# Kernel tuning notes

Hardware: AMD Instinct MI355X
Metric: run time of the kernel (lower is better)

## Reference

```python
import jax, jax.numpy as jnp
import numpy as np

N2 = 128      # time horizon (days)
M = 16384     # number of regions / batched chains
START = 6     # seeding window (days with externally seeded cases)


def setup_inputs() -> dict:
    key = jax.random.key(0)
    k0, k1, k2, k3, k4 = jax.random.split(key, 5)
    # reproduction numbers R_t in [0, 2)
    rt = jax.random.uniform(k0, (N2, M), dtype=jnp.float32) * 2.0
    deaths_gt = jax.random.uniform(k1, (N2, M), dtype=jnp.float32)
    # serial-interval distribution (positive, sums to 1 so the recurrence stays bounded)
    si_raw = jax.random.uniform(k2, (N2,), dtype=jnp.float32)
    SI = si_raw / jnp.sum(si_raw)
    f_raw = jax.random.uniform(k3, (N2, M), dtype=jnp.float32)
    f = f_raw / jnp.sum(f_raw, axis=0, keepdims=True) * 0.01
    # seeded cases for the first START days
    seed = jax.random.uniform(k4, (START, M), dtype=jnp.float32)
    return {"rt": rt, "deaths_gt": deaths_gt, "SI": SI, "f": f,
            "seed": seed, "start": START}


def _predict_cases(rt, SI, seed, start):
    # prediction[i, m] = rt[i, m] * sum_{j < i} prediction[j, m] * SI[i - j]
    # sequential triangular recurrence over time -> lax.scan with full carry.
    n2, m = rt.shape
    idx = jnp.arange(n2)
    pred0 = jnp.zeros((n2, m), rt.dtype).at[:start].set(seed)

    def step(pred, i):
        d = i - idx                                   # SI lag for each j
        w = jnp.where(d > 0, SI[jnp.clip(d, 0, n2 - 1)], 0.0)  # [N2], zero for j >= i
        conv = w @ pred                               # [M]
        row = jnp.where(i >= start, rt[i] * conv, pred[i])
        return pred.at[i].set(row), None

    pred, _ = jax.lax.scan(step, pred0, jnp.arange(n2))
    return pred


def _predict_deaths(pred, f, start):
    # E_deaths[i, m] = sum_{j <= i-2} pred[j, m] * f[i-j, m]
    # = causal per-region convolution with lags d = i-j >= 2 (so zero f[0], f[1]).
    n2, m = pred.shape
    f_eff = f.at[:2].set(0.0)
    conv = jax.vmap(lambda p, k: jnp.convolve(p, k)[:n2],
                    in_axes=1, out_axes=1)(pred, f_eff)   # [N2, M]
    i = jnp.arange(n2)[:, None]
    # rows before `start` are untouched by the loop (0), row 0 is set to 1e-9
    return jnp.where(i >= start, conv, jnp.where(i == 0, 1e-9, 0.0))


def reference(rt, deaths_gt, SI, f, seed, start):
    cases_pred = _predict_cases(rt, SI, seed, start)
    deaths_pred = _predict_deaths(cases_pred, f, start)
    return jnp.mean((deaths_pred - deaths_gt) ** 2)  # nn.MSELoss
```

## Files before the change

### kernel.cpp

```cpp
#include <hip/hip_runtime.h>

#define N2 128
#define MM 16384
#define START 6
#define TC 64
#define W 8
#define BT (TC * W)


__global__ __launch_bounds__(BT) void npi_fused(
    const float* __restrict__ rt, const float* __restrict__ dgt,
    const float* __restrict__ si, const float* __restrict__ f,
    const float* __restrict__ seed, float* __restrict__ out)
{
    __shared__ float predT[N2 * TC];
    __shared__ float red[8 * 16 * TC];
    float* si_s = &red[7 * 16 * TC];
    float* lred = &red[7 * 16 * TC + N2];

    const int t = threadIdx.x;
    const int c = t & 63;
    const int w = t >> 6;
    const int m = blockIdx.x * TC + c;

    if (t < N2) si_s[t] = si[t];
    __syncthreads();

    float sr[16];
#pragma unroll
    for (int k = 1; k < 16; ++k) sr[k] = si_s[k];

    if (w == 7) {
        float v[16];
#pragma unroll
        for (int k = 0; k < 16; ++k) {
            if (k < START) {
                v[k] = seed[k * MM + m];
            } else {
                float s = 0.f;
#pragma unroll
                for (int kk = 0; kk < 16; ++kk)
                    if (kk < k) s += v[kk] * sr[k - kk];
                v[k] = rt[k * MM + m] * s;
            }
            predT[k * TC + c] = v[k];
        }
    }
    __syncthreads();

    for (int b = 1; b < 8; ++b) {
        const int i0 = b << 4;
        float r16[16];
        if (w == 7) {
#pragma unroll
            for (int k = 0; k < 16; ++k) r16[k] = rt[(i0 + k) * MM + m];
        } else if (w < b) {
            const int j0 = w << 4;
            const int D0 = i0 - j0 - 15;
            float c16[16];
#pragma unroll
            for (int e = 0; e < 16; ++e) c16[(e + 1) & 15] = si_s[D0 + e];
            float acc[16];
#pragma unroll
            for (int k = 0; k < 16; ++k) acc[k] = 0.f;
#pragma unroll
            for (int s = 0; s < 16; ++s) {
                float p = predT[((j0 + 15 - s) << 6) + c];
#pragma unroll
                for (int k = 0; k < 16; ++k)
                    acc[k] += p * c16[(s + k + 1) & 15];
                if (s < 15) c16[(s + 1) & 15] = si_s[D0 + 16 + s];
            }
#pragma unroll
            for (int k = 0; k < 16; ++k)
                red[(((w << 4) + k) << 6) + c] = acc[k];
        }
        __syncthreads();

#pragma unroll
        for (int e2 = 0; e2 < 2; ++e2) {
            int e = t + (e2 << 9);
            int k = e >> 6, c2 = e & 63;
            float tot = 0.f;
            for (int ww = 0; ww < b; ++ww)
                tot += red[(((ww << 4) + k) << 6) + c2];
            predT[((i0 + k) << 6) + c2] = tot;
        }
        __syncthreads();

        if (w == 7) {
            float v[16];
#pragma unroll
            for (int k = 0; k < 16; ++k) {
                float s = predT[((i0 + k) << 6) + c];
#pragma unroll
                for (int kk = 0; kk < 16; ++kk)
                    if (kk < k) s += v[kk] * sr[k - kk];
                v[k] = r16[k] * s;
                predT[((i0 + k) << 6) + c] = v[k];
            }
        }
        __syncthreads();
    }

#pragma unroll
    for (int q = 0; q < 16; ++q) {
        int d = w + (q << 3);
        red[(d << 6) + c] = f[d * MM + m];
    }
    __syncthreads();

    float lsum = 0.f;
    if (w == 0) {
        float d0 = 1e-9f - dgt[m];
        lsum = d0 * d0;
#pragma unroll
        for (int i = 1; i < START; ++i) {
            float di = dgt[i * MM + m];
            lsum += di * di;
        }
    }

#pragma unroll
    for (int half = 0; half < 2; ++half) {
        const int n = half ? (15 - w) : w;
        const int i0 = START + (n << 3);
        float acc8[8];
#pragma unroll
        for (int k = 0; k < 8; ++k) acc8[k] = 0.f;

        const int J = (i0 - 1) & ~7;
        const int jend = (i0 + 5 < 125) ? (i0 + 5) : 125;
        for (int j = J; j <= jend; ++j) {
            float pv = predT[(j << 6) + c];
#pragma unroll
            for (int k = 0; k < 8; ++k) {
                int d = i0 + k - j;
                if (d >= 2 && (i0 + k) < N2)
                    acc8[k] += pv * red[(d << 6) + c];
            }
        }
        if (J > 0) {
            float c8[8];
            const int d0f = i0 - J + 1;
#pragma unroll
            for (int k = 0; k < 8; ++k) c8[k] = red[((d0f + k) << 6) + c];
            for (int j8 = J - 8; j8 >= 0; j8 -= 8) {
                const int dbase = i0 - j8 - 7;
#pragma unroll
                for (int s = 0; s < 8; ++s) {
                    float pv = predT[((j8 + 7 - s) << 6) + c];
#pragma unroll
                    for (int k = 0; k < 8; ++k)
                        acc8[k] += pv * c8[(s + k) & 7];
                    int dr = dbase + s + 8;
                    if (dr > N2 - 1) dr = N2 - 1;
                    c8[s] = red[(dr << 6) + c];
                }
            }
        }
#pragma unroll
        for (int k = 0; k < 8; ++k) {
            int i = i0 + k;
            if (i < N2) {
                float diff = acc8[k] - dgt[i * MM + m];
                lsum += diff * diff;
            }
        }
    }

#pragma unroll
    for (int off = 32; off > 0; off >>= 1)
        lsum += __shfl_down(lsum, off, 64);
    __syncthreads();
    if (c == 0) lred[w] = lsum;
    __syncthreads();
    if (t == 0) {
        float tot = 0.f;
#pragma unroll
        for (int ww = 0; ww < W; ++ww) tot += lred[ww];
        atomicAdd(out, tot * (1.0f / ((float)N2 * (float)MM)));
    }
}

extern "C" void kernel_launch(void* const* d_in, const int* in_sizes, int n_in,
                              void* d_out, int out_size, void* d_ws, size_t ws_size,
                              hipStream_t stream) {
    const float* rt   = (const float*)d_in[0];
    const float* dgt  = (const float*)d_in[1];
    const float* si   = (const float*)d_in[2];
    const float* f    = (const float*)d_in[3];
    const float* seed = (const float*)d_in[4];

    hipMemsetAsync(d_out, 0, sizeof(float), stream);
    npi_fused<<<dim3(MM / TC), dim3(BT), 0, stream>>>(
        rt, dgt, si, f, seed, (float*)d_out);
}
```

Before: 109.5 us.

## Shrink block to 16 columns with padded LDS and split death conv across lanes

After: 116.3 us. +6.2%, slower.

```diff
diff --git a/kernel.cpp b/kernel.cpp
--- a/kernel.cpp
+++ b/kernel.cpp
@@ -3,47 +3,99 @@
 #define N2 128
 #define MM 16384
 #define START 6
-#define TC 64
-#define W 8
-#define BT (TC * W)
-
-
-__global__ __launch_bounds__(BT) void npi_fused(
+#define TC 16
+#define BT 256
+#define PST 17
+
+__device__ __forceinline__ void conv_chunk(int i0, int odd, int c,
+                                           const float* __restrict__ predT,
+                                           const float* __restrict__ fT,
+                                           float acc[8]) {
+#pragma unroll
+    for (int k = 0; k < 8; ++k) acc[k] = 0.f;
+    const int J = (i0 - 1) & ~7;
+    const int Jmid = (J >> 1) & ~7;
+    int jtop, jbot;
+    if (odd) {
+        const int jend = (i0 + 5 < 125) ? (i0 + 5) : 125;
+        for (int j = J; j <= jend; ++j) {
+            float pv = predT[j * PST + c];
+#pragma unroll
+            for (int k = 0; k < 8; ++k) {
+                int d = i0 + k - j;
+                if (d >= 2 && (i0 + k) < N2)
+                    acc[k] += pv * fT[d * PST + c];
+            }
+        }
+        jtop = J;  jbot = Jmid;
+    } else {
+        jtop = Jmid; jbot = 0;
+    }
+    if (jtop > jbot) {
+        float c8[8];
+        const int d0f = i0 - jtop + 1;
+#pragma unroll
+        for (int k = 0; k < 8; ++k) c8[k] = fT[(d0f + k) * PST + c];
+        for (int j8 = jtop - 8; j8 >= jbot; j8 -= 8) {
+            const int dbase = i0 - j8 - 7;
+#pragma unroll
+            for (int s = 0; s < 8; ++s) {
+                float pv = predT[(j8 + 7 - s) * PST + c];
+#pragma unroll
+                for (int k = 0; k < 8; ++k)
+                    acc[k] += pv * c8[(s + k) & 7];
+                int dr = dbase + s + 8;
+                if (dr > N2 - 1) dr = N2 - 1;
+                c8[s] = fT[dr * PST + c];
+            }
+        }
+    }
+}
+
+__global__ __launch_bounds__(BT, 4) void npi_fused(
     const float* __restrict__ rt, const float* __restrict__ dgt,
     const float* __restrict__ si, const float* __restrict__ f,
     const float* __restrict__ seed, float* __restrict__ out)
 {
-    __shared__ float predT[N2 * TC];
-    __shared__ float red[8 * 16 * TC];
-    float* si_s = &red[7 * 16 * TC];
-    float* lred = &red[7 * 16 * TC + N2];
+    __shared__ float predT[N2 * PST];
+    __shared__ float fT[N2 * PST];
+    __shared__ float red[7 * 16 * PST];
+    __shared__ float si_s[N2];
+    __shared__ float lred[4];
 
     const int t = threadIdx.x;
-    const int c = t & 63;
-    const int w = t >> 6;
+    const int c = t & 15;
+    const int vw = t >> 4;
     const int m = blockIdx.x * TC + c;
 
+#pragma unroll
+    for (int q = 0; q < 8; ++q) {
+        int d = (q << 4) + vw;
+        fT[d * PST + c] = f[d * MM + m];
+    }
     if (t < N2) si_s[t] = si[t];
+    if (vw < START) predT[vw * PST + c] = seed[vw * MM + m];
+    else if (vw < 16) red[vw * PST + c] = rt[vw * MM + m];
     __syncthreads();
 
     float sr[16];
 #pragma unroll
     for (int k = 1; k < 16; ++k) sr[k] = si_s[k];
 
-    if (w == 7) {
+    if (vw == 15) {
         float v[16];
 #pragma unroll
         for (int k = 0; k < 16; ++k) {
             if (k < START) {
-                v[k] = seed[k * MM + m];
+                v[k] = predT[k * PST + c];
             } else {
                 float s = 0.f;
 #pragma unroll
                 for (int kk = 0; kk < 16; ++kk)
                     if (kk < k) s += v[kk] * sr[k - kk];
-                v[k] = rt[k * MM + m] * s;
-            }
-            predT[k * TC + c] = v[k];
+                v[k] = red[k * PST + c] * s;
+                predT[k * PST + c] = v[k];
+            }
         }
     }
     __syncthreads();
@@ -51,11 +103,11 @@
     for (int b = 1; b < 8; ++b) {
         const int i0 = b << 4;
         float r16[16];
-        if (w == 7) {
+        if (vw == 15) {
 #pragma unroll
             for (int k = 0; k < 16; ++k) r16[k] = rt[(i0 + k) * MM + m];
-        } else if (w < b) {
-            const int j0 = w << 4;
+        } else if (vw < b) {
+            const int j0 = vw << 4;
             const int D0 = i0 - j0 - 15;
             float c16[16];
 #pragma unroll
@@ -65,7 +117,7 @@
             for (int k = 0; k < 16; ++k) acc[k] = 0.f;
 #pragma unroll
             for (int s = 0; s < 16; ++s) {
-                float p = predT[((j0 + 15 - s) << 6) + c];
+                float p = predT[(j0 + 15 - s) * PST + c];
 #pragma unroll
                 for (int k = 0; k < 16; ++k)
                     acc[k] += p * c16[(s + k + 1) & 15];
@@ -73,112 +125,75 @@
             }
 #pragma unroll
             for (int k = 0; k < 16; ++k)
-                red[(((w << 4) + k) << 6) + c] = acc[k];
+                red[((vw << 4) + k) * PST + c] = acc[k];
         }
         __syncthreads();
 
-#pragma unroll
-        for (int e2 = 0; e2 < 2; ++e2) {
-            int e = t + (e2 << 9);
-            int k = e >> 6, c2 = e & 63;
+        {
             float tot = 0.f;
-            for (int ww = 0; ww < b; ++ww)
-                tot += red[(((ww << 4) + k) << 6) + c2];
-            predT[((i0 + k) << 6) + c2] = tot;
+            for (int w2 = 0; w2 < b; ++w2)
+                tot += red[((w2 << 4) + vw) * PST + c];
+            predT[(i0 + vw) * PST + c] = tot;
         }
         __syncthreads();
 
-        if (w == 7) {
+        if (vw == 15) {
+            float h[16];
+#pragma unroll
+            for (int k = 0; k < 16; ++k) h[k] = predT[(i0 + k) * PST + c];
             float v[16];
 #pragma unroll
             for (int k = 0; k < 16; ++k) {
-                float s = predT[((i0 + k) << 6) + c];
+                float s = h[k];
 #pragma unroll
                 for (int kk = 0; kk < 16; ++kk)
                     if (kk < k) s += v[kk] * sr[k - kk];
                 v[k] = r16[k] * s;
-                predT[((i0 + k) << 6) + c] = v[k];
+                predT[(i0 + k) * PST + c] = v[k];
             }
         }
         __syncthreads();
     }
 
-#pragma unroll
-    for (int q = 0; q < 16; ++q) {
-        int d = w + (q << 3);
-        red[(d << 6) + c] = f[d * MM + m];
-    }
-    __syncthreads();
-
     float lsum = 0.f;
-    if (w == 0) {
-        float d0 = 1e-9f - dgt[m];
+    if (vw >= 8 && vw < 8 + START) {
+        int i = vw - 8;
+        float di = dgt[i * MM + m];
+        float d0 = (i == 0) ? (1e-9f - di) : di;
         lsum = d0 * d0;
-#pragma unroll
-        for (int i = 1; i < START; ++i) {
-            float di = dgt[i * MM + m];
-            lsum += di * di;
-        }
-    }
-
-#pragma unroll
-    for (int half = 0; half < 2; ++half) {
-        const int n = half ? (15 - w) : w;
-        const int i0 = START + (n << 3);
-        float acc8[8];
-#pragma unroll
-        for (int k = 0; k < 8; ++k) acc8[k] = 0.f;
-
-        const int J = (i0 - 1) & ~7;
-        const int jend = (i0 + 5 < 125) ? (i0 + 5) : 125;
-        for (int j = J; j <= jend; ++j) {
-            float pv = predT[(j << 6) + c];
-#pragma unroll
-            for (int k = 0; k < 8; ++k) {
-                int d = i0 + k - j;
-                if (d >= 2 && (i0 + k) < N2)
-                    acc8[k] += pv * red[(d << 6) + c];
-            }
-        }
-        if (J > 0) {
-            float c8[8];
-            const int d0f = i0 - J + 1;
-#pragma unroll
-            for (int k = 0; k < 8; ++k) c8[k] = red[((d0f + k) << 6) + c];
-            for (int j8 = J - 8; j8 >= 0; j8 -= 8) {
-                const int dbase = i0 - j8 - 7;
-#pragma unroll
-                for (int s = 0; s < 8; ++s) {
-                    float pv = predT[((j8 + 7 - s) << 6) + c];
-#pragma unroll
-                    for (int k = 0; k < 8; ++k)
-                        acc8[k] += pv * c8[(s + k) & 7];
-                    int dr = dbase + s + 8;
-                    if (dr > N2 - 1) dr = N2 - 1;
-                    c8[s] = red[(dr << 6) + c];
-                }
-            }
-        }
-#pragma unroll
-        for (int k = 0; k < 8; ++k) {
-            int i = i0 + k;
-            if (i < N2) {
-                float diff = acc8[k] - dgt[i * MM + m];
-                lsum += diff * diff;
-            }
+    }
+
+    const int p = vw >> 1;
+    const int odd = vw & 1;
+    const int i0a = START + (p << 3);
+    const int i0b = START + ((15 - p) << 3);
+    float accA[8], accB[8];
+    conv_chunk(i0a, odd, c, predT, fT, accA);
+    conv_chunk(i0b, odd, c, predT, fT, accB);
+
+#pragma unroll
+    for (int k = 0; k < 8; ++k) {
+        accA[k] += __shfl_xor(accA[k], 16, 64);
+        accB[k] += __shfl_xor(accB[k], 16, 64);
+    }
+    const int i0o = odd ? i0b : i0a;
+#pragma unroll
+    for (int k = 0; k < 8; ++k) {
+        int i = i0o + k;
+        if (i < N2) {
+            float av = odd ? accB[k] : accA[k];
+            float diff = av - dgt[i * MM + m];
+            lsum += diff * diff;
         }
     }
 
 #pragma unroll
     for (int off = 32; off > 0; off >>= 1)
         lsum += __shfl_down(lsum, off, 64);
-    __syncthreads();
-    if (c == 0) lred[w] = lsum;
+    if ((t & 63) == 0) lred[t >> 6] = lsum;
     __syncthreads();
     if (t == 0) {
-        float tot = 0.f;
-#pragma unroll
-        for (int ww = 0; ww < W; ++ww) tot += lred[ww];
+        float tot = lred[0] + lred[1] + lred[2] + lred[3];
         atomicAdd(out, tot * (1.0f / ((float)N2 * (float)MM)));
     }
 }
```

## Split recurrence work across 8 thread groups per 32 columns with balanced lag ranges

Applied to the files above, without the earlier changes.

Result: faster. 105.9 us (-3.3%).

```diff
diff --git a/kernel.cpp b/kernel.cpp
--- a/kernel.cpp
+++ b/kernel.cpp
@@ -3,168 +3,194 @@
 #define N2 128
 #define MM 16384
 #define START 6
-#define TC 64
-#define W 8
-#define BT (TC * W)
-
-
-__global__ __launch_bounds__(BT) void npi_fused(
+#define CB 32
+#define BT 256
+#define PROWS 136
+#define FROWS 152
+
+__global__ __launch_bounds__(BT, 2) void npi_fused(
     const float* __restrict__ rt, const float* __restrict__ dgt,
     const float* __restrict__ si, const float* __restrict__ f,
     const float* __restrict__ seed, float* __restrict__ out)
 {
-    __shared__ float predT[N2 * TC];
-    __shared__ float red[8 * 16 * TC];
-    float* si_s = &red[7 * 16 * TC];
-    float* lred = &red[7 * 16 * TC + N2];
+    __shared__ float predT[PROWS * CB];
+    __shared__ float fTd[FROWS * CB];
+    __shared__ float part[4 * 16 * CB];
+    __shared__ float si_s[N2];
+    __shared__ float lred[4];
 
     const int t = threadIdx.x;
-    const int c = t & 63;
+    const int c = t & (CB - 1);
     const int w = t >> 6;
-    const int m = blockIdx.x * TC + c;
+    const int g = t >> 5;
+    const int hw = g & 1;
+    const int m = blockIdx.x * CB + c;
+
+    float fregs[16];
+#pragma unroll
+    for (int q = 0; q < 16; ++q)
+        fregs[q] = f[((g << 4) + q) * MM + m];
 
     if (t < N2) si_s[t] = si[t];
+    if (g < START) predT[(g << 5) + c] = seed[g * MM + m];
+    predT[((128 + g) << 5) + c] = 0.f;
+    fTd[(g << 5) + c] = 0.f;
+    fTd[((8 + g) << 5) + c] = 0.f;
+    if (g < 2) fTd[((16 + g) << 5) + c] = 0.f;
+    fTd[((144 + g) << 5) + c] = 0.f;
+
+    float r16v[16];
+#pragma unroll
+    for (int k = 0; k < 16; ++k)
+        r16v[k] = rt[k * MM + m];
+
     __syncthreads();
 
     float sr[16];
 #pragma unroll
     for (int k = 1; k < 16; ++k) sr[k] = si_s[k];
 
-    if (w == 7) {
+    {
         float v[16];
 #pragma unroll
         for (int k = 0; k < 16; ++k) {
             if (k < START) {
-                v[k] = seed[k * MM + m];
+                v[k] = predT[(k << 5) + c];
             } else {
                 float s = 0.f;
 #pragma unroll
                 for (int kk = 0; kk < 16; ++kk)
                     if (kk < k) s += v[kk] * sr[k - kk];
-                v[k] = rt[k * MM + m] * s;
-            }
-            predT[k * TC + c] = v[k];
+                v[k] = r16v[k] * s;
+            }
+        }
+        if (w == 3 && hw == 0) {
+#pragma unroll
+            for (int k = START; k < 16; ++k) predT[(k << 5) + c] = v[k];
         }
     }
     __syncthreads();
 
     for (int b = 1; b < 8; ++b) {
         const int i0 = b << 4;
-        float r16[16];
-        if (w == 7) {
-#pragma unroll
-            for (int k = 0; k < 16; ++k) r16[k] = rt[(i0 + k) * MM + m];
-        } else if (w < b) {
-            const int j0 = w << 4;
-            const int D0 = i0 - j0 - 15;
-            float c16[16];
-#pragma unroll
-            for (int e = 0; e < 16; ++e) c16[(e + 1) & 15] = si_s[D0 + e];
-            float acc[16];
-#pragma unroll
-            for (int k = 0; k < 16; ++k) acc[k] = 0.f;
-#pragma unroll
-            for (int s = 0; s < 16; ++s) {
-                float p = predT[((j0 + 15 - s) << 6) + c];
+        const int nst = b << 1;
+#pragma unroll
+        for (int k = 0; k < 16; ++k)
+            r16v[k] = rt[(i0 + k) * MM + m];
+
+        const int jhi = nst * (g + 1);
+        const int base = i0 - jhi + 1;
+        float c16[16];
+#pragma unroll
+        for (int e = 0; e < 16; ++e) c16[e] = si_s[base + e];
+        float acc[16];
+#pragma unroll
+        for (int k = 0; k < 16; ++k) acc[k] = 0.f;
+#pragma unroll
+        for (int u = 0; u < 14; ++u) {
+            if (u < nst) {
+                float p = predT[((jhi - 1 - u) << 5) + c];
 #pragma unroll
                 for (int k = 0; k < 16; ++k)
-                    acc[k] += p * c16[(s + k + 1) & 15];
-                if (s < 15) c16[(s + 1) & 15] = si_s[D0 + 16 + s];
-            }
+                    acc[k] += p * c16[(u + k) & 15];
+                if (u + 1 < nst) c16[u] = si_s[base + 16 + u];
+            }
+        }
+#pragma unroll
+        for (int k = 0; k < 16; ++k)
+            acc[k] += __shfl_xor(acc[k], 32, 64);
+        if (hw == 0) {
 #pragma unroll
             for (int k = 0; k < 16; ++k)
-                red[(((w << 4) + k) << 6) + c] = acc[k];
+                part[(((w << 4) + k) << 5) + c] = acc[k];
         }
         __syncthreads();
 
-#pragma unroll
-        for (int e2 = 0; e2 < 2; ++e2) {
-            int e = t + (e2 << 9);
-            int k = e >> 6, c2 = e & 63;
-            float tot = 0.f;
-            for (int ww = 0; ww < b; ++ww)
-                tot += red[(((ww << 4) + k) << 6) + c2];
-            predT[((i0 + k) << 6) + c2] = tot;
+        float v[16];
+#pragma unroll
+        for (int k = 0; k < 16; ++k) {
+            float s = part[(k << 5) + c] + part[((16 + k) << 5) + c]
+                    + part[((32 + k) << 5) + c] + part[((48 + k) << 5) + c];
+#pragma unroll
+            for (int kk = 0; kk < 16; ++kk)
+                if (kk < k) s += v[kk] * sr[k - kk];
+            v[k] = r16v[k] * s;
+        }
+        {
+            float a0, a1;
+            if (w == 0)      { a0 = hw ? v[2]  : v[0];  a1 = hw ? v[3]  : v[1];  }
+            else if (w == 1) { a0 = hw ? v[6]  : v[4];  a1 = hw ? v[7]  : v[5];  }
+            else if (w == 2) { a0 = hw ? v[10] : v[8];  a1 = hw ? v[11] : v[9];  }
+            else             { a0 = hw ? v[14] : v[12]; a1 = hw ? v[15] : v[13]; }
+            const int r0 = i0 + (w << 2) + (hw << 1);
+            predT[(r0 << 5) + c] = a0;
+            predT[((r0 + 1) << 5) + c] = a1;
         }
         __syncthreads();
-
-        if (w == 7) {
-            float v[16];
+    }
+
+#pragma unroll
+    for (int q = 0; q < 16; ++q) {
+        int d = (g << 4) + q;
+        fTd[((16 + d) << 5) + c] = (d < 2) ? 0.f : fregs[q];
+    }
+    __syncthreads();
+
+    float lsum = 0.f;
+    if (hw == 0) {
+        float dv = dgt[w * MM + m];
+        float e0 = (w == 0) ? (1e-9f - dv) : dv;
+        lsum += e0 * e0;
+        if (w < 2) {
+            float d2 = dgt[(4 + w) * MM + m];
+            lsum += d2 * d2;
+        }
+    }
+
+#pragma unroll
+    for (int half = 0; half < 2; ++half) {
+        const int n = half ? (7 - w) : w;
+        const int i0 = START + (n << 4);
+        const int jhi2 = i0 + 14;
+        const int steps = jhi2 >> 1;
+        const int jh = hw ? jhi2 : (jhi2 >> 1);
+        const int fb = 17 + i0 - jh;
+
+        float dg[16];
+#pragma unroll
+        for (int k = 0; k < 16; ++k)
+            dg[k] = (i0 + k < N2) ? dgt[(i0 + k) * MM + m] : 0.f;
+
+        float cf[16];
+#pragma unroll
+        for (int e = 0; e < 16; ++e) cf[e] = fTd[((fb + e) << 5) + c];
+        float acc[16];
+#pragma unroll
+        for (int k = 0; k < 16; ++k) acc[k] = 0.f;
+
+        for (int sb = 0; sb < steps; sb += 16) {
+#pragma unroll
+            for (int u = 0; u < 16; ++u) {
+                int s = sb + u;
+                if (s < steps) {
+                    float p = predT[((jh - 1 - s) << 5) + c];
+#pragma unroll
+                    for (int k = 0; k < 16; ++k)
+                        acc[k] += p * cf[(u + k) & 15];
+                    cf[u] = fTd[((fb + 16 + s) << 5) + c];
+                }
+            }
+        }
+#pragma unroll
+        for (int k = 0; k < 16; ++k)
+            acc[k] += __shfl_xor(acc[k], 32, 64);
+        if (hw == 0) {
 #pragma unroll
             for (int k = 0; k < 16; ++k) {
-                float s = predT[((i0 + k) << 6) + c];
-#pragma unroll
-                for (int kk = 0; kk < 16; ++kk)
-                    if (kk < k) s += v[kk] * sr[k - kk];
-                v[k] = r16[k] * s;
-                predT[((i0 + k) << 6) + c] = v[k];
-            }
-        }
-        __syncthreads();
-    }
-
-#pragma unroll
-    for (int q = 0; q < 16; ++q) {
-        int d = w + (q << 3);
-        red[(d << 6) + c] = f[d * MM + m];
-    }
-    __syncthreads();
-
-    float lsum = 0.f;
-    if (w == 0) {
-        float d0 = 1e-9f - dgt[m];
-        lsum = d0 * d0;
-#pragma unroll
-        for (int i = 1; i < START; ++i) {
-            float di = dgt[i * MM + m];
-            lsum += di * di;
-        }
-    }
-
-#pragma unroll
-    for (int half = 0; half < 2; ++half) {
-        const int n = half ? (15 - w) : w;
-        const int i0 = START + (n << 3);
-        float acc8[8];
-#pragma unroll
-        for (int k = 0; k < 8; ++k) acc8[k] = 0.f;
-
-        const int J = (i0 - 1) & ~7;
-        const int jend = (i0 + 5 < 125) ? (i0 + 5) : 125;
-        for (int j = J; j <= jend; ++j) {
-            float pv = predT[(j << 6) + c];
-#pragma unroll
-            for (int k = 0; k < 8; ++k) {
-                int d = i0 + k - j;
-                if (d >= 2 && (i0 + k) < N2)
-                    acc8[k] += pv * red[(d << 6) + c];
-            }
-        }
-        if (J > 0) {
-            float c8[8];
-            const int d0f = i0 - J + 1;
-#pragma unroll
-            for (int k = 0; k < 8; ++k) c8[k] = red[((d0f + k) << 6) + c];
-            for (int j8 = J - 8; j8 >= 0; j8 -= 8) {
-                const int dbase = i0 - j8 - 7;
-#pragma unroll
-                for (int s = 0; s < 8; ++s) {
-                    float pv = predT[((j8 + 7 - s) << 6) + c];
-#pragma unroll
-                    for (int k = 0; k < 8; ++k)
-                        acc8[k] += pv * c8[(s + k) & 7];
-                    int dr = dbase + s + 8;
-                    if (dr > N2 - 1) dr = N2 - 1;
-                    c8[s] = red[(dr << 6) + c];
+                if (i0 + k < N2) {
+                    float diff = acc[k] - dg[k];
+                    lsum += diff * diff;
                 }
-            }
-        }
-#pragma unroll
-        for (int k = 0; k < 8; ++k) {
-            int i = i0 + k;
-            if (i < N2) {
-                float diff = acc8[k] - dgt[i * MM + m];
-                lsum += diff * diff;
             }
         }
     }
@@ -172,15 +198,11 @@
 #pragma unroll
     for (int off = 32; off > 0; off >>= 1)
         lsum += __shfl_down(lsum, off, 64);
-    __syncthreads();
-    if (c == 0) lred[w] = lsum;
-    __syncthreads();
-    if (t == 0) {
-        float tot = 0.f;
-#pragma unroll
-        for (int ww = 0; ww < W; ++ww) tot += lred[ww];
-        atomicAdd(out, tot * (1.0f / ((float)N2 * (float)MM)));
-    }
+    if ((t & 63) == 0) lred[w] = lsum;
+    __syncthreads();
+    if (t == 0)
+        atomicAdd(out, (lred[0] + lred[1] + lred[2] + lred[3]) *
+                       (1.0f / ((float)N2 * (float)MM)));
 }
 
 extern "C" void kernel_launch(void* const* d_in, const int* in_sizes, int n_in,
@@ -193,6 +215,6 @@
     const float* seed = (const float*)d_in[4];
 
     hipMemsetAsync(d_out, 0, sizeof(float), stream);
-    npi_fused<<<dim3(MM / TC), dim3(BT), 0, stream>>>(
+    npi_fused<<<dim3(MM / CB), dim3(BT), 0, stream>>>(
         rt, dgt, si, f, seed, (float*)d_out);
 }
```
